# Performance work log

Hardware: AMD Instinct MI355X
Metric: run time of the kernel (lower is better)

## Reference

```python
import jax, jax.numpy as jnp
import numpy as np

B, Hh, Ww, E = 8, 32, 32, 256
HEADS = 8
KD = E // HEADS  # 32
FFN = 1024
NQ = 64
SCALING = KD ** -0.5
EPS = 1e-6


def _ln(x, g, b):
    m = x.mean(-1, keepdims=True)
    v = ((x - m) ** 2).mean(-1, keepdims=True)
    return (x - m) * jax.lax.rsqrt(v + EPS) * g + b


def _dwconv(x, w, b, pad):
    # x: (b,h,w,c); w: (c,1,kh,kw) depthwise
    y = jnp.transpose(x, (0, 3, 1, 2))
    y = jax.lax.conv_general_dilated(
        y, w, (1, 1), [(pad, pad), (pad, pad)],
        dimension_numbers=('NCHW', 'OIHW', 'NCHW'),
        feature_group_count=y.shape[1])
    y = y + b[None, :, None, None]
    return jnp.transpose(y, (0, 2, 3, 1))


def _rot2(x):
    x1 = x[..., ::2]
    x2 = x[..., 1::2]
    return jnp.stack([-x2, x1], axis=-1).reshape(x.shape)


def _theta_shift(x, sin, cos):
    return x * cos + _rot2(x) * sin


def _ffn(x, fc1_w, fc1_b, fc2_w, fc2_b):
    h = jax.nn.gelu(x @ fc1_w.T + fc1_b, approximate=False)
    return h @ fc2_w.T + fc2_b


def _mha(q, k, v, in_w, in_b, out_w, out_b):
    # torch nn.MultiheadAttention, batch_first=True
    wq, wk, wv = in_w[:E], in_w[E:2 * E], in_w[2 * E:]
    bq, bk, bv = in_b[:E], in_b[E:2 * E], in_b[2 * E:]
    b_, nq, _ = q.shape
    lk = k.shape[1]
    qp = (q @ wq.T + bq).reshape(b_, nq, HEADS, KD).transpose(0, 2, 1, 3)
    kp = (k @ wk.T + bk).reshape(b_, lk, HEADS, KD).transpose(0, 2, 1, 3)
    vp = (v @ wv.T + bv).reshape(b_, lk, HEADS, KD).transpose(0, 2, 1, 3)
    att = jax.nn.softmax(jnp.einsum('bhqd,bhkd->bhqk', qp, kp) * SCALING, axis=-1)
    out = jnp.einsum('bhqk,bhkd->bhqd', att, vp)
    out = out.transpose(0, 2, 1, 3).reshape(b_, nq, E)
    return out @ out_w.T + out_b


def setup_inputs() -> dict:
    key = jax.random.key(0)
    ks = jax.random.split(key, 24)
    n = lambda i, shp, s=1.0: jax.random.normal(ks[i], shp, jnp.float32) * s
    W = 0.02
    return {
        'x': n(0, (B, Hh, Ww, E)),
        'queries': n(1, (B, NQ, E)),
        'sin': n(2, (Hh, Ww, KD)),
        'cos': n(3, (Hh, Ww, KD)),
        'mask': n(4, (HEADS, Hh * Ww, Hh * Ww)),
        'ln1_g': jnp.ones((E,), jnp.float32), 'ln1_b': jnp.zeros((E,), jnp.float32),
        'ln2_g': jnp.ones((E,), jnp.float32), 'ln2_b': jnp.zeros((E,), jnp.float32),
        'wq': n(5, (E, E), W), 'bq': jnp.zeros((E,), jnp.float32),
        'wk': n(6, (E, E), W), 'bk': jnp.zeros((E,), jnp.float32),
        'wv': n(7, (E, E), W), 'bv': jnp.zeros((E,), jnp.float32),
        'lepe_w': n(8, (E, 1, 5, 5), W), 'lepe_b': jnp.zeros((E,), jnp.float32),
        'wo': n(9, (E, E), W), 'bo': jnp.zeros((E,), jnp.float32),
        'fc1_w': n(10, (FFN, E), W), 'fc1_b': jnp.zeros((FFN,), jnp.float32),
        'fc2_w': n(11, (E, FFN), W), 'fc2_b': jnp.zeros((E,), jnp.float32),
        'pos_w': n(12, (E, 1, 3, 3), W), 'pos_b': jnp.zeros((E,), jnp.float32),
        'ca_in_w': n(13, (3 * E, E), W), 'ca_in_b': jnp.zeros((3 * E,), jnp.float32),
        'ca_out_w': n(14, (E, E), W), 'ca_out_b': jnp.zeros((E,), jnp.float32),
    }


def reference(x, queries, sin, cos, mask, ln1_g, ln1_b, ln2_g, ln2_b,
              wq, bq, wk, bk, wv, bv, lepe_w, lepe_b, wo, bo,
              fc1_w, fc1_b, fc2_w, fc2_b, pos_w, pos_b,
              ca_in_w, ca_in_b, ca_out_w, ca_out_b):
    # conditional positional encoding
    x = x + _dwconv(x, pos_w, pos_b, 1)

    # --- retention branch (VisionRetentionAll) ---
    hn = _ln(x, ln1_g, ln1_b)
    q = hn @ wq.T + bq
    k = (hn @ wk.T + bk) * SCALING
    v = hn @ wv.T + bv
    lepe = _dwconv(v, lepe_w, lepe_b, 2)
    b_, hh, ww, _ = x.shape
    L = hh * ww
    qh = q.reshape(b_, hh, ww, HEADS, KD).transpose(0, 3, 1, 2, 4)
    kh = k.reshape(b_, hh, ww, HEADS, KD).transpose(0, 3, 1, 2, 4)
    qr = _theta_shift(qh, sin, cos).reshape(b_, HEADS, L, KD)
    kr = _theta_shift(kh, sin, cos).reshape(b_, HEADS, L, KD)
    vr = v.reshape(b_, hh, ww, HEADS, KD).transpose(0, 3, 1, 2, 4).reshape(b_, HEADS, L, KD)
    att = jax.nn.softmax(jnp.einsum('bnqd,bnkd->bnqk', qr, kr) + mask, axis=-1)
    out = jnp.einsum('bnqk,bnkd->bnqd', att, vr)
    out = out.transpose(0, 2, 1, 3).reshape(b_, hh, ww, E) + lepe
    x = x + (out @ wo.T + bo)

    # --- FFN branch ---
    x = x + _ffn(_ln(x, ln2_g, ln2_b), fc1_w, fc1_b, fc2_w, fc2_b)

    # --- cross-attention on queries ---
    xs = x.reshape(b_, L, E)
    q_ln = _ln(queries, ln1_g, ln1_b)
    queries = queries + _mha(q_ln, xs, xs, ca_in_w, ca_in_b, ca_out_w, ca_out_b)
    queries = queries + _ffn(_ln(queries, ln2_g, ln2_b), fc1_w, fc1_b, fc2_w, fc2_b)
    return x, queries
```

## Files before the change

kernel.cpp:

```cpp
#include <hip/hip_runtime.h>
#include <hip/hip_bf16.h>

#define B_      8
#define HH      32
#define WW      32
#define E_      256
#define HEADS_  8
#define KD_     32
#define FFN_    1024
#define NQ_     64
#define L_      1024
#define SCALING_ 0.17677669529663687f
#define LOG2E_  1.44269504088896340736f
#define EPS_    1e-6f

typedef short bf16x8 __attribute__((ext_vector_type(8)));
typedef float f32x4 __attribute__((ext_vector_type(4)));
typedef unsigned short ushort_t;

#if __has_builtin(__builtin_amdgcn_exp2f)
#define EXP2(x) __builtin_amdgcn_exp2f(x)
#else
#define EXP2(x) exp2f(x)
#endif

__device__ __forceinline__ ushort_t f2bf(float f) {
    __hip_bfloat16 h = __float2bfloat16(f);
    return *reinterpret_cast<ushort_t*>(&h);
}
__device__ __forceinline__ unsigned int pk2(float a, float b) {
    __hip_bfloat162 h = __float22bfloat162_rn(float2{a, b});
    return *reinterpret_cast<unsigned int*>(&h);
}

__global__ __launch_bounds__(256) void posconv_ln2(
        const float* __restrict__ x, const float* __restrict__ PWT,
        const float* __restrict__ bias, const float* __restrict__ g,
        const float* __restrict__ bb, float* __restrict__ X, ushort_t* __restrict__ HN) {
    int tid = threadIdx.x;
    int wave = tid >> 6, lane = tid & 63;
    int b = blockIdx.x >> 8, rem = blockIdx.x & 255;
    int hh = rem >> 3, wg = rem & 7;
    int ww = wg * 4 + wave;
    int e = lane * 4;
    long row = ((long)(b * HH + hh)) * WW + ww;

    float4 bi = *reinterpret_cast<const float4*>(bias + e);
    float ax = bi.x, ay = bi.y, az = bi.z, aw = bi.w;
#pragma unroll
    for (int dh = 0; dh < 3; ++dh) {
        int h2 = hh + dh - 1; if (h2 < 0 || h2 >= HH) continue;
        float rx = 0.f, ry = 0.f, rz = 0.f, rw = 0.f;
#pragma unroll
        for (int dw = 0; dw < 3; ++dw) {
            int w2 = ww + dw - 1; if (w2 < 0 || w2 >= WW) continue;
            float4 v = *reinterpret_cast<const float4*>(x + (((long)(b * HH + h2)) * WW + w2) * E_ + e);
            float4 wt = *reinterpret_cast<const float4*>(PWT + (dh * 3 + dw) * 256 + e);
            rx += v.x * wt.x; ry += v.y * wt.y; rz += v.z * wt.z; rw += v.w * wt.w;
        }
        ax += rx; ay += ry; az += rz; aw += rw;
    }
    float4 x4 = *reinterpret_cast<const float4*>(x + row * E_ + e);
    float vx = x4.x + ax, vy = x4.y + ay, vz = x4.z + az, vw = x4.w + aw;
    float4 o4 = {vx, vy, vz, vw};
    *reinterpret_cast<float4*>(X + row * E_ + e) = o4;

    float s = vx + vy + vz + vw;
#pragma unroll
    for (int off = 1; off < 64; off <<= 1) s += __shfl_xor(s, off);
    float mean = s * (1.0f / E_);
    float dx = vx - mean, dy = vy - mean, dz = vz - mean, dw_ = vw - mean;
    float s2 = dx * dx + dy * dy + dz * dz + dw_ * dw_;
#pragma unroll
    for (int off = 1; off < 64; off <<= 1) s2 += __shfl_xor(s2, off);
    float r = rsqrtf(s2 * (1.0f / E_) + EPS_);
    float4 g4 = *reinterpret_cast<const float4*>(g + e);
    float4 b4 = *reinterpret_cast<const float4*>(bb + e);
    uint2 p;
    p.x = pk2(dx * r * g4.x + b4.x, dy * r * g4.y + b4.y);
    p.y = pk2(dz * r * g4.z + b4.z, dw_ * r * g4.w + b4.w);
    *reinterpret_cast<uint2*>(HN + row * E_ + e) = p;
}

__global__ __launch_bounds__(256) void lepe2(
        const float* __restrict__ v, const float* __restrict__ LWT,
        const float* __restrict__ bias, float* __restrict__ out) {
    int tid = threadIdx.x;
    int wave = tid >> 6, lane = tid & 63;
    int b = blockIdx.x >> 8, rem = blockIdx.x & 255;
    int hh = rem >> 3, wg = rem & 7;
    int ww = wg * 4 + wave;
    int e = lane * 4;
    long row = ((long)(b * HH + hh)) * WW + ww;

    float4 bi = *reinterpret_cast<const float4*>(bias + e);
    float ax = bi.x, ay = bi.y, az = bi.z, aw = bi.w;
#pragma unroll
    for (int dh = 0; dh < 5; ++dh) {
        int h2 = hh + dh - 2; if (h2 < 0 || h2 >= HH) continue;
        float rx = 0.f, ry = 0.f, rz = 0.f, rw = 0.f;
#pragma unroll
        for (int dw = 0; dw < 5; ++dw) {
            int w2 = ww + dw - 2; if (w2 < 0 || w2 >= WW) continue;
            float4 vv = *reinterpret_cast<const float4*>(v + (((long)(b * HH + h2)) * WW + w2) * E_ + e);
            float4 wt = *reinterpret_cast<const float4*>(LWT + (dh * 5 + dw) * 256 + e);
            rx += vv.x * wt.x; ry += vv.y * wt.y; rz += vv.z * wt.z; rw += vv.w * wt.w;
        }
        ax += rx; ay += ry; az += rz; aw += rw;
    }
    float4 o4 = {ax, ay, az, aw};
    *reinterpret_cast<float4*>(out + row * E_ + e) = o4;
}

__global__ __launch_bounds__(256) void ln2(
        const float* __restrict__ x, const float* __restrict__ g,
        const float* __restrict__ b, ushort_t* __restrict__ y) {
    int tid = threadIdx.x;
    int wave = tid >> 6, lane = tid & 63;
    long row = (long)blockIdx.x * 4 + wave;
    int e = lane * 4;
    float4 v4 = *reinterpret_cast<const float4*>(x + row * E_ + e);
    float s = v4.x + v4.y + v4.z + v4.w;
#pragma unroll
    for (int off = 1; off < 64; off <<= 1) s += __shfl_xor(s, off);
    float mean = s * (1.0f / E_);
    float dx = v4.x - mean, dy = v4.y - mean, dz = v4.z - mean, dw = v4.w - mean;
    float s2 = dx * dx + dy * dy + dz * dz + dw * dw;
#pragma unroll
    for (int off = 1; off < 64; off <<= 1) s2 += __shfl_xor(s2, off);
    float r = rsqrtf(s2 * (1.0f / E_) + EPS_);
    float4 g4 = *reinterpret_cast<const float4*>(g + e);
    float4 b4 = *reinterpret_cast<const float4*>(b + e);
    uint2 p;
    p.x = pk2(dx * r * g4.x + b4.x, dy * r * g4.y + b4.y);
    p.y = pk2(dz * r * g4.z + b4.z, dw * r * g4.w + b4.w);
    *reinterpret_cast<uint2*>(y + row * E_ + e) = p;
}

struct WTab { const float* src[8]; };
__global__ void wconv_kernel(WTab t, ushort_t* __restrict__ dst,
                             const float* __restrict__ lepe_w, const float* __restrict__ pos_w,
                             float* __restrict__ LWT, float* __restrict__ PWT) {
    if (blockIdx.x == 1024) {
        int e = threadIdx.x;
#pragma unroll
        for (int tp = 0; tp < 25; ++tp) LWT[tp * 256 + e] = lepe_w[e * 25 + tp];
#pragma unroll
        for (int tp = 0; tp < 9; ++tp) PWT[tp * 256 + e] = pos_w[e * 9 + tp];
        return;
    }
    const int off[9] = {0, 65536, 131072, 196608, 262144, 524288, 786432, 983040, 1048576};
    long base = ((long)blockIdx.x * 256 + threadIdx.x) * 4;
    int r = 0;
#pragma unroll
    for (int i = 1; i < 8; ++i) r = (base >= off[i]) ? i : r;
    const float* s =
        r == 0 ? t.src[0] : r == 1 ? t.src[1] : r == 2 ? t.src[2] : r == 3 ? t.src[3] :
        r == 4 ? t.src[4] : r == 5 ? t.src[5] : r == 6 ? t.src[6] : t.src[7];
    float4 v = *reinterpret_cast<const float4*>(s + (base - off[r]));
    uint2 p;
    p.x = pk2(v.x, v.y);
    p.y = pk2(v.z, v.w);
    *reinterpret_cast<uint2*>(dst + base) = p;
}

template<int ACT, int THETA>
__global__ __launch_bounds__(256) void gemm2(
        const ushort_t* __restrict__ A, const ushort_t* __restrict__ W,
        const float* __restrict__ bias, ushort_t* __restrict__ Cb,
        float* __restrict__ Cf, const float* __restrict__ resid,
        int M, int N, int K, float scale, int scaleN,
        const float* __restrict__ sinp, const float* __restrict__ cosp) {
    __shared__ __align__(16) ushort_t As[64 * 72];
    __shared__ __align__(16) ushort_t Ws[64 * 72];
    int tid = threadIdx.x;
    int wave = tid >> 6, lane = tid & 63;
    int quad = lane >> 4, l16 = lane & 15;
    int wm = wave >> 1, wn = wave & 1;
    long mBase = (long)blockIdx.x * 64;
    long nBase = (long)blockIdx.y * 64;
    int row = tid >> 3, q = tid & 7;
    int row2 = (tid + 256) >> 3, q2 = (tid + 256) & 7;

    f32x4 acc[2][2];
#pragma unroll
    for (int i = 0; i < 2; ++i)
#pragma unroll
        for (int j = 0; j < 2; ++j) acc[i][j] = (f32x4){0.f, 0.f, 0.f, 0.f};

    int nT = K >> 6;
    uint4 a0 = *reinterpret_cast<const uint4*>(A + (mBase + row) * (long)K + q * 8);
    uint4 a1 = *reinterpret_cast<const uint4*>(A + (mBase + row2) * (long)K + q2 * 8);
    uint4 w0 = *reinterpret_cast<const uint4*>(W + (nBase + row) * (long)K + q * 8);
    uint4 w1 = *reinterpret_cast<const uint4*>(W + (nBase + row2) * (long)K + q2 * 8);

    for (int t = 0; t < nT; ++t) {
        *reinterpret_cast<uint4*>(&As[row * 72 + q * 8]) = a0;
        *reinterpret_cast<uint4*>(&As[row2 * 72 + q2 * 8]) = a1;
        *reinterpret_cast<uint4*>(&Ws[row * 72 + q * 8]) = w0;
        *reinterpret_cast<uint4*>(&Ws[row2 * 72 + q2 * 8]) = w1;
        __syncthreads();
        if (t + 1 < nT) {
            int kt = (t + 1) << 6;
            a0 = *reinterpret_cast<const uint4*>(A + (mBase + row) * (long)K + kt + q * 8);
            a1 = *reinterpret_cast<const uint4*>(A + (mBase + row2) * (long)K + kt + q2 * 8);
            w0 = *reinterpret_cast<const uint4*>(W + (nBase + row) * (long)K + kt + q * 8);
            w1 = *reinterpret_cast<const uint4*>(W + (nBase + row2) * (long)K + kt + q2 * 8);
        }
#pragma unroll
        for (int kk = 0; kk < 2; ++kk) {
            bf16x8 af[2], bfr[2];
#pragma unroll
            for (int i = 0; i < 2; ++i)
                af[i] = *reinterpret_cast<const bf16x8*>(&As[(wm * 32 + i * 16 + l16) * 72 + kk * 32 + quad * 8]);
#pragma unroll
            for (int j = 0; j < 2; ++j)
                bfr[j] = *reinterpret_cast<const bf16x8*>(&Ws[(wn * 32 + j * 16 + l16) * 72 + kk * 32 + quad * 8]);
#pragma unroll
            for (int i = 0; i < 2; ++i)
#pragma unroll
                for (int j = 0; j < 2; ++j)
                    acc[i][j] = __builtin_amdgcn_mfma_f32_16x16x32_bf16(af[i], bfr[j], acc[i][j], 0, 0, 0);
        }
        __syncthreads();
    }

#pragma unroll
    for (int i = 0; i < 2; ++i)
#pragma unroll
        for (int j = 0; j < 2; ++j) {
            long n = nBase + wn * 32 + j * 16 + l16;
            float bn = bias[n];
            float eff = (n < scaleN) ? scale : 1.0f;
#pragma unroll
            for (int r = 0; r < 4; ++r) {
                long m = mBase + wm * 32 + i * 16 + quad * 4 + r;
                float v = (acc[i][j][r] + bn) * eff;
                if (THETA) {
                    float other = __shfl_xor(v, 1);
                    int l = (int)(m & (L_ - 1));
                    int d = (int)(n & 31);
                    float cc = cosp[l * 32 + d], ss = sinp[l * 32 + d];
                    v = v * cc + ((n & 1) ? other : -other) * ss;
                }
                if (ACT) v = 0.5f * v * (1.0f + erff(v * 0.70710678118654752f));
                if (resid) v += resid[m * N + n];
                if (Cf) Cf[m * N + n] = v;
                if (Cb) Cb[m * N + n] = f2bf(v);
            }
        }
}

__global__ __launch_bounds__(256) void gemm_qkv3(
        const ushort_t* __restrict__ A, const ushort_t* __restrict__ WB,
        const float* __restrict__ bq, const float* __restrict__ bk, const float* __restrict__ bv,
        ushort_t* __restrict__ Qb, ushort_t* __restrict__ Kb, ushort_t* __restrict__ Vb,
        float* __restrict__ Vbf, const float* __restrict__ sinp,
        const float* __restrict__ cosp, float kscl) {
    __shared__ __align__(16) ushort_t As[64 * 72];
    __shared__ __align__(16) ushort_t Ws[64 * 72];
    int tid = threadIdx.x;
    int wave = tid >> 6, lane = tid & 63;
    int quad = lane >> 4, l16 = lane & 15;
    int wm = wave >> 1, wn = wave & 1;
    long mBase = (long)blockIdx.x * 64;
    int sel = blockIdx.y >> 2;
    int nLocBase = (blockIdx.y & 3) * 64;
    const ushort_t* W = WB + ((long)(sel * 256 + nLocBase)) * 256;
    const float* bias = sel == 0 ? bq : (sel == 1 ? bk : bv);
    const int K = 256;
    int row = tid >> 3, q = tid & 7;
    int row2 = (tid + 256) >> 3, q2 = (tid + 256) & 7;

    f32x4 acc[2][2];
#pragma unroll
    for (int i = 0; i < 2; ++i)
#pragma unroll
        for (int j = 0; j < 2; ++j) acc[i][j] = (f32x4){0.f, 0.f, 0.f, 0.f};

    uint4 a0 = *reinterpret_cast<const uint4*>(A + (mBase + row) * (long)K + q * 8);
    uint4 a1 = *reinterpret_cast<const uint4*>(A + (mBase + row2) * (long)K + q2 * 8);
    uint4 w0 = *reinterpret_cast<const uint4*>(W + row * (long)K + q * 8);
    uint4 w1 = *reinterpret_cast<const uint4*>(W + row2 * (long)K + q2 * 8);

    for (int t = 0; t < 4; ++t) {
        *reinterpret_cast<uint4*>(&As[row * 72 + q * 8]) = a0;
        *reinterpret_cast<uint4*>(&As[row2 * 72 + q2 * 8]) = a1;
        *reinterpret_cast<uint4*>(&Ws[row * 72 + q * 8]) = w0;
        *reinterpret_cast<uint4*>(&Ws[row2 * 72 + q2 * 8]) = w1;
        __syncthreads();
        if (t < 3) {
            int kt = (t + 1) << 6;
            a0 = *reinterpret_cast<const uint4*>(A + (mBase + row) * (long)K + kt + q * 8);
            a1 = *reinterpret_cast<const uint4*>(A + (mBase + row2) * (long)K + kt + q2 * 8);
            w0 = *reinterpret_cast<const uint4*>(W + row * (long)K + kt + q * 8);
            w1 = *reinterpret_cast<const uint4*>(W + row2 * (long)K + kt + q2 * 8);
        }
#pragma unroll
        for (int kk = 0; kk < 2; ++kk) {
            bf16x8 af[2], bfr[2];
#pragma unroll
            for (int i = 0; i < 2; ++i)
                af[i] = *reinterpret_cast<const bf16x8*>(&As[(wm * 32 + i * 16 + l16) * 72 + kk * 32 + quad * 8]);
#pragma unroll
            for (int j = 0; j < 2; ++j)
                bfr[j] = *reinterpret_cast<const bf16x8*>(&Ws[(wn * 32 + j * 16 + l16) * 72 + kk * 32 + quad * 8]);
#pragma unroll
            for (int i = 0; i < 2; ++i)
#pragma unroll
                for (int j = 0; j < 2; ++j)
                    acc[i][j] = __builtin_amdgcn_mfma_f32_16x16x32_bf16(af[i], bfr[j], acc[i][j], 0, 0, 0);
        }
        __syncthreads();
    }

    ushort_t* Cb = sel == 0 ? Qb : (sel == 1 ? Kb : Vb);
#pragma unroll
    for (int i = 0; i < 2; ++i)
#pragma unroll
        for (int j = 0; j < 2; ++j) {
            int n = nLocBase + wn * 32 + j * 16 + l16;
            float bn = bias[n];
#pragma unroll
            for (int r = 0; r < 4; ++r) {
                long m = mBase + wm * 32 + i * 16 + quad * 4 + r;
                float v = acc[i][j][r] + bn;
                if (sel == 1) v *= kscl;
                if (sel < 2) {
                    float other = __shfl_xor(v, 1);
                    int l = (int)(m & (L_ - 1));
                    int d = n & 31;
                    float cc = cosp[l * 32 + d], ss = sinp[l * 32 + d];
                    v = v * cc + ((n & 1) ? other : -other) * ss;
                }
                Cb[m * 256 + n] = f2bf(v);
                if (sel == 2) Vbf[m * 256 + n] = v;
            }
        }
}

__global__ __launch_bounds__(256) void attn5(
        const ushort_t* __restrict__ Q, int qs,
        const ushort_t* __restrict__ K, int ks,
        const ushort_t* __restrict__ V, int vs,
        const float* __restrict__ maskf,
        const float* __restrict__ lepe, ushort_t* __restrict__ out, int nq) {
    __shared__ __align__(16) ushort_t Vt[2][32 * 136];
    __shared__ __align__(16) ushort_t Pl[4][16 * 136];
    int tid = threadIdx.x;
    int wave = tid >> 6, lane = tid & 63;
    int quad = lane >> 4, l16 = lane & 15;
    int qt = blockIdx.x, h = blockIdx.y, b = blockIdx.z;
    int qbase = qt * 64 + wave * 16;

    bf16x8 qfrag = *reinterpret_cast<const bf16x8*>(
        Q + ((long)b * nq + qbase + l16) * qs + h * KD_ + quad * 8);

    f32x4 acc_o[2];
    acc_o[0] = (f32x4){0.f, 0.f, 0.f, 0.f};
    acc_o[1] = (f32x4){0.f, 0.f, 0.f, 0.f};
    float lsum[4] = {0.f, 0.f, 0.f, 0.f};

    int kp = tid & 63;
    int dq = tid >> 6;

    const ushort_t* vp = V + ((long)b * L_ + 2 * kp) * vs + h * KD_ + dq * 8;
    uint4 ua = *reinterpret_cast<const uint4*>(vp);
    uint4 ub = *reinterpret_cast<const uint4*>(vp + vs);
    {
        const unsigned int* wa = reinterpret_cast<const unsigned int*>(&ua);
        const unsigned int* wb = reinterpret_cast<const unsigned int*>(&ub);
#pragma unroll
        for (int i = 0; i < 8; ++i) {
            unsigned int x16 = (wa[i >> 1] >> ((i & 1) * 16)) & 0xFFFF;
            unsigned int y16 = (wb[i >> 1] >> ((i & 1) * 16)) & 0xFFFF;
            *reinterpret_cast<unsigned int*>(&Vt[0][(dq * 8 + i) * 136 + 2 * kp]) =
                x16 | (y16 << 16);
        }
    }

    for (int it = 0; it < 8; ++it) {
        int kb = it * 128;
        __syncthreads();
        if (it < 7) {
            const ushort_t* vn = V + ((long)b * L_ + kb + 128 + 2 * kp) * vs + h * KD_ + dq * 8;
            ua = *reinterpret_cast<const uint4*>(vn);
            ub = *reinterpret_cast<const uint4*>(vn + vs);
        }

#pragma unroll
        for (int g = 0; g < 2; ++g) {
            bf16x8 kf[4];
            float mr[4][4];
#pragma unroll
            for (int kt4 = 0; kt4 < 4; ++kt4)
                kf[kt4] = *reinterpret_cast<const bf16x8*>(
                    K + ((long)b * L_ + kb + (g * 4 + kt4) * 16 + l16) * ks + h * KD_ + quad * 8);
            if (maskf) {
#pragma unroll
                for (int kt4 = 0; kt4 < 4; ++kt4)
#pragma unroll
                    for (int r = 0; r < 4; ++r)
                        mr[kt4][r] = maskf[((long)h * L_ + qbase + quad * 4 + r) * L_ +
                                           kb + (g * 4 + kt4) * 16 + l16];
            }
#pragma unroll
            for (int kt4 = 0; kt4 < 4; ++kt4) {
                int kcol = (g * 4 + kt4) * 16;
                f32x4 sa = (f32x4){0.f, 0.f, 0.f, 0.f};
                sa = __builtin_amdgcn_mfma_f32_16x16x32_bf16(qfrag, kf[kt4], sa, 0, 0, 0);
#pragma unroll
                for (int r = 0; r < 4; ++r) {
                    float s = maskf ? fmaf(mr[kt4][r], LOG2E_, sa[r]) : sa[r];
                    float p = EXP2(s);
                    lsum[r] += p;
                    Pl[wave][(quad * 4 + r) * 136 + kcol + l16] = f2bf(p);
                }
            }
        }

#pragma unroll
        for (int c = 0; c < 4; ++c) {
            bf16x8 pa = *reinterpret_cast<const bf16x8*>(
                &Pl[wave][l16 * 136 + c * 32 + quad * 8]);
#pragma unroll
            for (int dt = 0; dt < 2; ++dt) {
                bf16x8 vf = *reinterpret_cast<const bf16x8*>(
                    &Vt[it & 1][(dt * 16 + l16) * 136 + c * 32 + quad * 8]);
                acc_o[dt] = __builtin_amdgcn_mfma_f32_16x16x32_bf16(pa, vf, acc_o[dt], 0, 0, 0);
            }
        }

        if (it < 7) {
            const unsigned int* wa = reinterpret_cast<const unsigned int*>(&ua);
            const unsigned int* wb = reinterpret_cast<const unsigned int*>(&ub);
#pragma unroll
            for (int i = 0; i < 8; ++i) {
                unsigned int x16 = (wa[i >> 1] >> ((i & 1) * 16)) & 0xFFFF;
                unsigned int y16 = (wb[i >> 1] >> ((i & 1) * 16)) & 0xFFFF;
                *reinterpret_cast<unsigned int*>(&Vt[(it + 1) & 1][(dq * 8 + i) * 136 + 2 * kp]) =
                    x16 | (y16 << 16);
            }
        }
    }

#pragma unroll
    for (int off = 1; off < 16; off <<= 1) {
#pragma unroll
        for (int r = 0; r < 4; ++r) lsum[r] += __shfl_xor(lsum[r], off);
    }

#pragma unroll
    for (int dt = 0; dt < 2; ++dt)
#pragma unroll
        for (int r = 0; r < 4; ++r) {
            float v = acc_o[dt][r] / lsum[r];
            long oi = ((long)b * nq + qbase + quad * 4 + r) * E_ + h * KD_ + dt * 16 + l16;
            if (lepe) v += lepe[oi];
            out[oi] = f2bf(v);
        }
}

extern "C" void kernel_launch(void* const* d_in, const int* in_sizes, int n_in,
                              void* d_out, int out_size, void* d_ws, size_t ws_size,
                              hipStream_t stream) {
    const float* x        = (const float*)d_in[0];
    const float* queries  = (const float*)d_in[1];
    const float* sinp     = (const float*)d_in[2];
    const float* cosp     = (const float*)d_in[3];
    const float* mask     = (const float*)d_in[4];
    const float* ln1_g    = (const float*)d_in[5];
    const float* ln1_b    = (const float*)d_in[6];
    const float* ln2_g    = (const float*)d_in[7];
    const float* ln2_b    = (const float*)d_in[8];
    const float* wq       = (const float*)d_in[9];
    const float* bq       = (const float*)d_in[10];
    const float* wk       = (const float*)d_in[11];
    const float* bk       = (const float*)d_in[12];
    const float* wv       = (const float*)d_in[13];
    const float* bv       = (const float*)d_in[14];
    const float* lepe_w   = (const float*)d_in[15];
    const float* lepe_b   = (const float*)d_in[16];
    const float* wo       = (const float*)d_in[17];
    const float* bo       = (const float*)d_in[18];
    const float* fc1_w    = (const float*)d_in[19];
    const float* fc1_b    = (const float*)d_in[20];
    const float* fc2_w    = (const float*)d_in[21];
    const float* fc2_b    = (const float*)d_in[22];
    const float* pos_w    = (const float*)d_in[23];
    const float* pos_b    = (const float*)d_in[24];
    const float* ca_in_w  = (const float*)d_in[25];
    const float* ca_in_b  = (const float*)d_in[26];
    const float* ca_out_w = (const float*)d_in[27];
    const float* ca_out_b = (const float*)d_in[28];

    float* ws = (float*)d_ws;
    const long SZ = (long)B_ * L_ * E_;
    float* X    = ws;
    float* Vbf  = ws + SZ;
    float* LEP  = ws + 2 * SZ;
    float* Q2   = LEP;
    ushort_t* U = (ushort_t*)(ws + 3 * SZ);
    ushort_t* T0    = U;
    ushort_t* Qb_u  = U + SZ;
    ushort_t* Kb_u  = U + 2 * SZ;
    ushort_t* Vb_u  = U + 3 * SZ;
    ushort_t* HID_u = U + 4 * SZ;
    ushort_t* WB    = U + 8 * SZ;
    float* LWT      = (float*)(WB + 1048576);
    float* PWT      = LWT + 6400;
    ushort_t* KV_u   = U + SZ;
    ushort_t* QLN_u  = Vb_u;
    ushort_t* QP_u   = Vb_u + 131072;
    ushort_t* CAO_u  = Vb_u + 262144;
    ushort_t* QHID_u = Vb_u + 393216;
    ushort_t* wqB    = WB;
    ushort_t* woB    = WB + 196608;
    ushort_t* fc1B   = WB + 262144;
    ushort_t* fc2B   = WB + 524288;
    ushort_t* cainB  = WB + 786432;
    ushort_t* caoutB = WB + 983040;

    float* XOUT = (float*)d_out;
    float* QOUT = (float*)d_out + 2097152;

    dim3 blk(256);
    const int rows = B_ * L_;
    const float* Z = nullptr;
    const float KSCL = SCALING_ * LOG2E_;

    WTab wt;
    wt.src[0] = wq; wt.src[1] = wk; wt.src[2] = wv; wt.src[3] = wo;
    wt.src[4] = fc1_w; wt.src[5] = fc2_w; wt.src[6] = ca_in_w; wt.src[7] = ca_out_w;

    wconv_kernel<<<1025, blk, 0, stream>>>(wt, WB, lepe_w, pos_w, LWT, PWT);
    posconv_ln2<<<2048, blk, 0, stream>>>(x, PWT, pos_b, ln1_g, ln1_b, X, T0);

    gemm_qkv3<<<dim3(128, 12), blk, 0, stream>>>(T0, wqB, bq, bk, bv, Qb_u, Kb_u, Vb_u,
                                                 Vbf, sinp, cosp, KSCL);
    lepe2<<<2048, blk, 0, stream>>>(Vbf, LWT, lepe_b, LEP);
    attn5<<<dim3(16, 8, 8), blk, 0, stream>>>(Qb_u, 256, Kb_u, 256, Vb_u, 256, mask, LEP, T0, L_);
    gemm2<0,0><<<dim3(128, 4), blk, 0, stream>>>(T0, woB, bo, nullptr, X, X, rows, 256, 256, 1.0f, 0, Z, Z);
    ln2<<<2048, blk, 0, stream>>>(X, ln2_g, ln2_b, T0);
    gemm2<1,0><<<dim3(128, 16), blk, 0, stream>>>(T0, fc1B, fc1_b, HID_u, nullptr, Z, rows, 1024, 256, 1.0f, 0, Z, Z);
    gemm2<0,0><<<dim3(128, 4), blk, 0, stream>>>(HID_u, fc2B, fc2_b, T0, XOUT, X, rows, 256, 1024, 1.0f, 0, Z, Z);

    ln2<<<128, blk, 0, stream>>>(queries, ln1_g, ln1_b, QLN_u);
    gemm2<0,0><<<dim3(8, 4), blk, 0, stream>>>(QLN_u, cainB, ca_in_b, QP_u, nullptr, Z, 512, 256, 256, 1.0f, 0, Z, Z);
    gemm2<0,0><<<dim3(128, 8), blk, 0, stream>>>(T0, cainB + 65536, ca_in_b + 256, KV_u, nullptr, Z, rows, 512, 256, KSCL, 256, Z, Z);
    attn5<<<dim3(1, 8, 8), blk, 0, stream>>>(QP_u, 256, KV_u, 512, KV_u + 256, 512, Z, Z, CAO_u, NQ_);
    gemm2<0,0><<<dim3(8, 4), blk, 0, stream>>>(CAO_u, caoutB, ca_out_b, nullptr, Q2, queries, 512, 256, 256, 1.0f, 0, Z, Z);
    ln2<<<128, blk, 0, stream>>>(Q2, ln2_g, ln2_b, QLN_u);
    gemm2<1,0><<<dim3(8, 16), blk, 0, stream>>>(QLN_u, fc1B, fc1_b, QHID_u, nullptr, Z, 512, 1024, 256, 1.0f, 0, Z, Z);
    gemm2<0,0><<<dim3(8, 4), blk, 0, stream>>>(QHID_u, fc2B, fc2_b, nullptr, QOUT, Q2, 512, 256, 1024, 1.0f, 0, Z, Z);
}
```

Before: 338.5 us.

## Split self-attention over key halves and fuse LePE conv into combine kernel

The self-attention kernel now splits the 1024 keys into two halves, launching 2048 blocks instead of 1024. Each block writes unnormalised fp32 partial outputs and row sums, and a new combine kernel merges the halves, normalises, and adds the depthwise LePE convolution computed inline. This removes the separate lepe kernel and its output round trip, and aims for more parallelism in attention. The cost is writing and rereading two fp32 partial tensors. The mask is also loaded up front for a whole 128-key tile.

```diff
diff --git a/kernel.cpp b/kernel.cpp
--- a/kernel.cpp
+++ b/kernel.cpp
@@ -80,36 +80,6 @@
     p.x = pk2(dx * r * g4.x + b4.x, dy * r * g4.y + b4.y);
     p.y = pk2(dz * r * g4.z + b4.z, dw_ * r * g4.w + b4.w);
     *reinterpret_cast<uint2*>(HN + row * E_ + e) = p;
-}
-
-__global__ __launch_bounds__(256) void lepe2(
-        const float* __restrict__ v, const float* __restrict__ LWT,
-        const float* __restrict__ bias, float* __restrict__ out) {
-    int tid = threadIdx.x;
-    int wave = tid >> 6, lane = tid & 63;
-    int b = blockIdx.x >> 8, rem = blockIdx.x & 255;
-    int hh = rem >> 3, wg = rem & 7;
-    int ww = wg * 4 + wave;
-    int e = lane * 4;
-    long row = ((long)(b * HH + hh)) * WW + ww;
-
-    float4 bi = *reinterpret_cast<const float4*>(bias + e);
-    float ax = bi.x, ay = bi.y, az = bi.z, aw = bi.w;
-#pragma unroll
-    for (int dh = 0; dh < 5; ++dh) {
-        int h2 = hh + dh - 2; if (h2 < 0 || h2 >= HH) continue;
-        float rx = 0.f, ry = 0.f, rz = 0.f, rw = 0.f;
-#pragma unroll
-        for (int dw = 0; dw < 5; ++dw) {
-            int w2 = ww + dw - 2; if (w2 < 0 || w2 >= WW) continue;
-            float4 vv = *reinterpret_cast<const float4*>(v + (((long)(b * HH + h2)) * WW + w2) * E_ + e);
-            float4 wt = *reinterpret_cast<const float4*>(LWT + (dh * 5 + dw) * 256 + e);
-            rx += vv.x * wt.x; ry += vv.y * wt.y; rz += vv.z * wt.z; rw += vv.w * wt.w;
-        }
-        ax += rx; ay += ry; az += rz; aw += rw;
-    }
-    float4 o4 = {ax, ay, az, aw};
-    *reinterpret_cast<float4*>(out + row * E_ + e) = o4;
 }
 
 __global__ __launch_bounds__(256) void ln2(
@@ -339,12 +309,176 @@
         }
 }
 
+__global__ __launch_bounds__(256) void attn6(
+        const ushort_t* __restrict__ Q, const ushort_t* __restrict__ K,
+        const ushort_t* __restrict__ V, const float* __restrict__ maskf,
+        float* __restrict__ PART0, float* __restrict__ PART1,
+        float* __restrict__ LS) {
+    __shared__ __align__(16) ushort_t Vt[2][32 * 136];
+    __shared__ __align__(16) ushort_t Pl[4][16 * 136];
+    int tid = threadIdx.x;
+    int wave = tid >> 6, lane = tid & 63;
+    int quad = lane >> 4, l16 = lane & 15;
+    int lin = blockIdx.x;
+    int t = lin & 127, inner = lin >> 7;
+    int h = t >> 4, qt = t & 15;
+    int b = inner >> 1, s = inner & 1;
+    int kb0 = s << 9;
+    int qbase = qt * 64 + wave * 16;
+
+    bf16x8 qfrag = *reinterpret_cast<const bf16x8*>(
+        Q + ((long)b * L_ + qbase + l16) * 256 + h * KD_ + quad * 8);
+
+    f32x4 acc_o[2];
+    acc_o[0] = (f32x4){0.f, 0.f, 0.f, 0.f};
+    acc_o[1] = (f32x4){0.f, 0.f, 0.f, 0.f};
+    float lsum[4] = {0.f, 0.f, 0.f, 0.f};
+
+    int kp = tid & 63;
+    int dq = tid >> 6;
+
+    const ushort_t* vp = V + ((long)b * L_ + kb0 + 2 * kp) * 256 + h * KD_ + dq * 8;
+    uint4 ua = *reinterpret_cast<const uint4*>(vp);
+    uint4 ub = *reinterpret_cast<const uint4*>(vp + 256);
+    {
+        const unsigned int* wa = reinterpret_cast<const unsigned int*>(&ua);
+        const unsigned int* wb = reinterpret_cast<const unsigned int*>(&ub);
+#pragma unroll
+        for (int i = 0; i < 8; ++i) {
+            unsigned int x16 = (wa[i >> 1] >> ((i & 1) * 16)) & 0xFFFF;
+            unsigned int y16 = (wb[i >> 1] >> ((i & 1) * 16)) & 0xFFFF;
+            *reinterpret_cast<unsigned int*>(&Vt[0][(dq * 8 + i) * 136 + 2 * kp]) =
+                x16 | (y16 << 16);
+        }
+    }
+
+    for (int it = 0; it < 4; ++it) {
+        int kb = kb0 + it * 128;
+        __syncthreads();
+        if (it < 3) {
+            const ushort_t* vn = V + ((long)b * L_ + kb + 128 + 2 * kp) * 256 + h * KD_ + dq * 8;
+            ua = *reinterpret_cast<const uint4*>(vn);
+            ub = *reinterpret_cast<const uint4*>(vn + 256);
+        }
+        float mr[8][4];
+#pragma unroll
+        for (int kt = 0; kt < 8; ++kt)
+#pragma unroll
+            for (int r = 0; r < 4; ++r)
+                mr[kt][r] = maskf[((long)h * L_ + qbase + quad * 4 + r) * L_ +
+                                  kb + kt * 16 + l16];
+
+#pragma unroll
+        for (int g = 0; g < 2; ++g) {
+            bf16x8 kf[4];
+#pragma unroll
+            for (int kt4 = 0; kt4 < 4; ++kt4)
+                kf[kt4] = *reinterpret_cast<const bf16x8*>(
+                    K + ((long)b * L_ + kb + (g * 4 + kt4) * 16 + l16) * 256 + h * KD_ + quad * 8);
+#pragma unroll
+            for (int kt4 = 0; kt4 < 4; ++kt4) {
+                int kt = g * 4 + kt4;
+                int kcol = kt * 16;
+                f32x4 sa = (f32x4){0.f, 0.f, 0.f, 0.f};
+                sa = __builtin_amdgcn_mfma_f32_16x16x32_bf16(qfrag, kf[kt4], sa, 0, 0, 0);
+#pragma unroll
+                for (int r = 0; r < 4; ++r) {
+                    float p = EXP2(fmaf(mr[kt][r], LOG2E_, sa[r]));
+                    lsum[r] += p;
+                    Pl[wave][(quad * 4 + r) * 136 + kcol + l16] = f2bf(p);
+                }
+            }
+        }
+
+#pragma unroll
+        for (int c = 0; c < 4; ++c) {
+            bf16x8 pa = *reinterpret_cast<const bf16x8*>(
+                &Pl[wave][l16 * 136 + c * 32 + quad * 8]);
+#pragma unroll
+            for (int dt = 0; dt < 2; ++dt) {
+                bf16x8 vf = *reinterpret_cast<const bf16x8*>(
+                    &Vt[it & 1][(dt * 16 + l16) * 136 + c * 32 + quad * 8]);
+                acc_o[dt] = __builtin_amdgcn_mfma_f32_16x16x32_bf16(pa, vf, acc_o[dt], 0, 0, 0);
+            }
+        }
+
+        if (it < 3) {
+            const unsigned int* wa = reinterpret_cast<const unsigned int*>(&ua);
+            const unsigned int* wb = reinterpret_cast<const unsigned int*>(&ub);
+#pragma unroll
+            for (int i = 0; i < 8; ++i) {
+                unsigned int x16 = (wa[i >> 1] >> ((i & 1) * 16)) & 0xFFFF;
+                unsigned int y16 = (wb[i >> 1] >> ((i & 1) * 16)) & 0xFFFF;
+                *reinterpret_cast<unsigned int*>(&Vt[(it + 1) & 1][(dq * 8 + i) * 136 + 2 * kp]) =
+                    x16 | (y16 << 16);
+            }
+        }
+    }
+
+#pragma unroll
+    for (int off = 1; off < 16; off <<= 1) {
+#pragma unroll
+        for (int r = 0; r < 4; ++r) lsum[r] += __shfl_xor(lsum[r], off);
+    }
+
+    float* P = s ? PART1 : PART0;
+#pragma unroll
+    for (int dt = 0; dt < 2; ++dt)
+#pragma unroll
+        for (int r = 0; r < 4; ++r)
+            P[((long)b * L_ + qbase + quad * 4 + r) * 256 + h * 32 + dt * 16 + l16] = acc_o[dt][r];
+    if (l16 == 0) {
+#pragma unroll
+        for (int r = 0; r < 4; ++r)
+            LS[(long)s * 65536 + ((long)b * L_ + qbase + quad * 4 + r) * 8 + h] = lsum[r];
+    }
+}
+
+__global__ __launch_bounds__(256) void combine2(
+        const float* __restrict__ P0, const float* __restrict__ P1,
+        const float* __restrict__ LS, const float* __restrict__ Vbf,
+        const float* __restrict__ LWT, const float* __restrict__ bias,
+        ushort_t* __restrict__ out) {
+    int tid = threadIdx.x;
+    int wave = tid >> 6, lane = tid & 63;
+    int b = blockIdx.x >> 8, rem = blockIdx.x & 255;
+    int hh = rem >> 3, wg = rem & 7;
+    int ww = wg * 4 + wave;
+    int e = lane * 4;
+    long row = ((long)(b * HH + hh)) * WW + ww;
+
+    float4 bi = *reinterpret_cast<const float4*>(bias + e);
+    float ax = bi.x, ay = bi.y, az = bi.z, aw = bi.w;
+#pragma unroll
+    for (int dh = 0; dh < 5; ++dh) {
+        int h2 = hh + dh - 2; if (h2 < 0 || h2 >= HH) continue;
+        float rx = 0.f, ry = 0.f, rz = 0.f, rw = 0.f;
+#pragma unroll
+        for (int dw = 0; dw < 5; ++dw) {
+            int w2 = ww + dw - 2; if (w2 < 0 || w2 >= WW) continue;
+            float4 vv = *reinterpret_cast<const float4*>(Vbf + (((long)(b * HH + h2)) * WW + w2) * E_ + e);
+            float4 wt = *reinterpret_cast<const float4*>(LWT + (dh * 5 + dw) * 256 + e);
+            rx += vv.x * wt.x; ry += vv.y * wt.y; rz += vv.z * wt.z; rw += vv.w * wt.w;
+        }
+        ax += rx; ay += ry; az += rz; aw += rw;
+    }
+
+    int h = e >> 5;
+    float l = LS[row * 8 + h] + LS[65536 + row * 8 + h];
+    float inv = 1.0f / l;
+    float4 p0 = *reinterpret_cast<const float4*>(P0 + row * 256 + e);
+    float4 p1 = *reinterpret_cast<const float4*>(P1 + row * 256 + e);
+    uint2 o;
+    o.x = pk2((p0.x + p1.x) * inv + ax, (p0.y + p1.y) * inv + ay);
+    o.y = pk2((p0.z + p1.z) * inv + az, (p0.w + p1.w) * inv + aw);
+    *reinterpret_cast<uint2*>(out + row * 256 + e) = o;
+}
+
 __global__ __launch_bounds__(256) void attn5(
         const ushort_t* __restrict__ Q, int qs,
         const ushort_t* __restrict__ K, int ks,
         const ushort_t* __restrict__ V, int vs,
-        const float* __restrict__ maskf,
-        const float* __restrict__ lepe, ushort_t* __restrict__ out, int nq) {
+        ushort_t* __restrict__ out, int nq) {
     __shared__ __align__(16) ushort_t Vt[2][32 * 136];
     __shared__ __align__(16) ushort_t Pl[4][16 * 136];
     int tid = threadIdx.x;
@@ -391,19 +525,10 @@
 #pragma unroll
         for (int g = 0; g < 2; ++g) {
             bf16x8 kf[4];
-            float mr[4][4];
 #pragma unroll
             for (int kt4 = 0; kt4 < 4; ++kt4)
                 kf[kt4] = *reinterpret_cast<const bf16x8*>(
                     K + ((long)b * L_ + kb + (g * 4 + kt4) * 16 + l16) * ks + h * KD_ + quad * 8);
-            if (maskf) {
-#pragma unroll
-                for (int kt4 = 0; kt4 < 4; ++kt4)
-#pragma unroll
-                    for (int r = 0; r < 4; ++r)
-                        mr[kt4][r] = maskf[((long)h * L_ + qbase + quad * 4 + r) * L_ +
-                                           kb + (g * 4 + kt4) * 16 + l16];
-            }
 #pragma unroll
             for (int kt4 = 0; kt4 < 4; ++kt4) {
                 int kcol = (g * 4 + kt4) * 16;
@@ -411,8 +536,7 @@
                 sa = __builtin_amdgcn_mfma_f32_16x16x32_bf16(qfrag, kf[kt4], sa, 0, 0, 0);
 #pragma unroll
                 for (int r = 0; r < 4; ++r) {
-                    float s = maskf ? fmaf(mr[kt4][r], LOG2E_, sa[r]) : sa[r];
-                    float p = EXP2(s);
+                    float p = EXP2(sa[r]);
                     lsum[r] += p;
                     Pl[wave][(quad * 4 + r) * 136 + kcol + l16] = f2bf(p);
                 }
@@ -456,7 +580,6 @@
         for (int r = 0; r < 4; ++r) {
             float v = acc_o[dt][r] / lsum[r];
             long oi = ((long)b * nq + qbase + quad * 4 + r) * E_ + h * KD_ + dt * 16 + l16;
-            if (lepe) v += lepe[oi];
             out[oi] = f2bf(v);
         }
 }
@@ -496,19 +619,21 @@
 
     float* ws = (float*)d_ws;
     const long SZ = (long)B_ * L_ * E_;
-    float* X    = ws;
-    float* Vbf  = ws + SZ;
-    float* LEP  = ws + 2 * SZ;
-    float* Q2   = LEP;
+    float* X     = ws;
+    float* Vbf   = ws + SZ;
+    float* PART1 = ws + 2 * SZ;
+    float* Q2    = PART1;
     ushort_t* U = (ushort_t*)(ws + 3 * SZ);
     ushort_t* T0    = U;
     ushort_t* Qb_u  = U + SZ;
     ushort_t* Kb_u  = U + 2 * SZ;
     ushort_t* Vb_u  = U + 3 * SZ;
     ushort_t* HID_u = U + 4 * SZ;
+    float* PART0    = (float*)HID_u;
     ushort_t* WB    = U + 8 * SZ;
     float* LWT      = (float*)(WB + 1048576);
     float* PWT      = LWT + 6400;
+    float* LS       = PWT + 2304;
     ushort_t* KV_u   = U + SZ;
     ushort_t* QLN_u  = Vb_u;
     ushort_t* QP_u   = Vb_u + 131072;
@@ -538,8 +663,8 @@
 
     gemm_qkv3<<<dim3(128, 12), blk, 0, stream>>>(T0, wqB, bq, bk, bv, Qb_u, Kb_u, Vb_u,
                                                  Vbf, sinp, cosp, KSCL);
-    lepe2<<<2048, blk, 0, stream>>>(Vbf, LWT, lepe_b, LEP);
-    attn5<<<dim3(16, 8, 8), blk, 0, stream>>>(Qb_u, 256, Kb_u, 256, Vb_u, 256, mask, LEP, T0, L_);
+    attn6<<<2048, blk, 0, stream>>>(Qb_u, Kb_u, Vb_u, mask, PART0, PART1, LS);
+    combine2<<<2048, blk, 0, stream>>>(PART0, PART1, LS, Vbf, LWT, lepe_b, T0);
     gemm2<0,0><<<dim3(128, 4), blk, 0, stream>>>(T0, woB, bo, nullptr, X, X, rows, 256, 256, 1.0f, 0, Z, Z);
     ln2<<<2048, blk, 0, stream>>>(X, ln2_g, ln2_b, T0);
     gemm2<1,0><<<dim3(128, 16), blk, 0, stream>>>(T0, fc1B, fc1_b, HID_u, nullptr, Z, rows, 1024, 256, 1.0f, 0, Z, Z);
@@ -548,7 +673,7 @@
     ln2<<<128, blk, 0, stream>>>(queries, ln1_g, ln1_b, QLN_u);
     gemm2<0,0><<<dim3(8, 4), blk, 0, stream>>>(QLN_u, cainB, ca_in_b, QP_u, nullptr, Z, 512, 256, 256, 1.0f, 0, Z, Z);
     gemm2<0,0><<<dim3(128, 8), blk, 0, stream>>>(T0, cainB + 65536, ca_in_b + 256, KV_u, nullptr, Z, rows, 512, 256, KSCL, 256, Z, Z);
-    attn5<<<dim3(1, 8, 8), blk, 0, stream>>>(QP_u, 256, KV_u, 512, KV_u + 256, 512, Z, Z, CAO_u, NQ_);
+    attn5<<<dim3(1, 8, 8), blk, 0, stream>>>(QP_u, 256, KV_u, 512, KV_u + 256, 512, CAO_u, NQ_);
     gemm2<0,0><<<dim3(8, 4), blk, 0, stream>>>(CAO_u, caoutB, ca_out_b, nullptr, Q2, queries, 512, 256, 256, 1.0f, 0, Z, Z);
     ln2<<<128, blk, 0, stream>>>(Q2, ln2_g, ln2_b, QLN_u);
     gemm2<1,0><<<dim3(8, 16), blk, 0, stream>>>(QLN_u, fc1B, fc1_b, QHID_u, nullptr, Z, 512, 1024, 256, 1.0f, 0, Z, Z);
```

After: 341.0 us. No clear change (+0.7%).
